# Performance work log

Measured on AMD Instinct MI355X. Metric: run time of the kernel, lower is better.

The kernel has to match this reference:

```python
import jax, jax.numpy as jnp
import numpy as np

N, K, CIN, COUT = 150000, 27, 128, 128


def setup_inputs() -> dict:
    key = jax.random.key(0)
    k1, k2, k3 = jax.random.split(key, 3)
    data = jax.random.normal(k1, (N, CIN), dtype=jnp.float32)
    weights = jax.random.normal(k2, (COUT, K, CIN), dtype=jnp.float32) * 0.05
    # neighbour indices in [-1, N): -1 marks empty octree neighbours (~1/151 here)
    neighbour = jax.random.randint(k3, (N, K), 0, N + 1, dtype=jnp.int64) - 1
    return {"data": data, "weights": weights, "neighbour": neighbour}


def reference(data, weights, neighbour):
    """Octree sparse conv: out[m] = sum_k W[:,k,:] @ data[neigh[m,k]] (0 if -1).

    Scans over the 27 kernel offsets so the [N,K,Cin] gather is never
    materialized; each step is a masked row-gather + dense GEMM.
    """
    w_k = jnp.transpose(weights, (1, 2, 0))   # [K, Cin, Cout]
    n_k = neighbour.T                          # [K, N]

    def body(acc, xs):
        w, idx = xs                            # [Cin, Cout], [N]
        valid = (idx >= 0)[:, None]            # [N, 1]
        g = jnp.where(valid, data[jnp.clip(idx, 0, None)], 0.0)  # [N, Cin]
        return acc + g @ w, None

    out0 = jnp.zeros((data.shape[0], w_k.shape[-1]), dtype=data.dtype)
    out, _ = jax.lax.scan(body, out0, (w_k, n_k))
    return out
```

## Files before the change

kernel.cpp:

```cpp
#include <hip/hip_runtime.h>

#define N_PTS 150000
#define NK 27
#define CIN 128
#define COUT 128
#define BM 256
#define NBLK ((N_PTS + BM - 1) / BM)

typedef __attribute__((ext_vector_type(8))) short bfrag8;
typedef __attribute__((ext_vector_type(4))) float facc4;

__device__ inline unsigned short f2bf(float f) {
    unsigned u = __builtin_bit_cast(unsigned, f);
    u += 0x7FFFu + ((u >> 16) & 1u);
    return (unsigned short)(u >> 16);
}
__device__ inline unsigned pack2(float a, float b) {
    return (unsigned)f2bf(a) | ((unsigned)f2bf(b) << 16);
}
__device__ inline void glds16(const void* g, void* l) {
    __builtin_amdgcn_global_load_lds(
        (const __attribute__((address_space(1))) void*)g,
        (__attribute__((address_space(3))) void*)l, 16, 0, 0);
}

__global__ void cast_data_kernel(const float* __restrict__ in,
                                 unsigned short* __restrict__ out) {
    const int n8_data = N_PTS * (CIN / 8);
    const int n8_all  = (N_PTS + 1) * (CIN / 8);
    int i = blockIdx.x * blockDim.x + threadIdx.x;
    int stride = gridDim.x * blockDim.x;
    for (; i < n8_all; i += stride) {
        uint4 v;
        if (i < n8_data) {
            const float4* p = (const float4*)(in + (size_t)i * 8);
            float4 x = p[0], y = p[1];
            v.x = pack2(x.x, x.y); v.y = pack2(x.z, x.w);
            v.z = pack2(y.x, y.y); v.w = pack2(y.z, y.w);
        } else {
            v.x = v.y = v.z = v.w = 0u;
        }
        *(uint4*)(out + (size_t)i * 8) = v;
    }
}

__global__ void prep_weights_h(const float* __restrict__ w,
                               unsigned short* __restrict__ wkh) {
    int i = blockIdx.x * blockDim.x + threadIdx.x;
    if (i >= NK * 2 * 128 * 8) return;
    int bu = i & 7, co = (i >> 3) & 127, h = (i >> 10) & 1, k = i >> 11;
    int ci = h * 64 + (bu ^ (co & 7)) * 8;
    const float4* src = (const float4*)(w + ((size_t)co * NK + k) * CIN + ci);
    float4 x = src[0], y = src[1];
    uint4 v;
    v.x = pack2(x.x, x.y); v.y = pack2(x.z, x.w);
    v.z = pack2(y.x, y.y); v.w = pack2(y.z, y.w);
    ((uint4*)wkh)[i] = v;
}


#define STAGE_A(Q, ADST)                                                     \
  {                                                                          \
    const int q_ = (Q);                                                      \
    const int k_ = q_ >> 1;                                                  \
    const int hb_ = (q_ & 1) << 7;                                           \
    int iv0 = *(const int*)(ldsI + i0base + k_ * 4);                         \
    int iv1 = *(const int*)(ldsI + i1base + k_ * 4);                         \
    size_t e0 = (r0ok && iv0 >= 0) ? (size_t)iv0 : (size_t)N_PTS;            \
    size_t e1 = (r1ok && iv1 >= 0) ? (size_t)iv1 : (size_t)N_PTS;            \
    glds16(dbfB + e0 * 256 + hb_ + aswz0, (ADST) + adst0);                   \
    glds16(dbfB + e1 * 256 + hb_ + aswz1, (ADST) + adst1);                   \
  }

#define STAGE_B(Q, BDST)                                                     \
    glds16(wkhB + (size_t)(Q) * 16384 + bsrc_c, (BDST) + bdst_lin);

#define MFMA_PHASE(ABUF, BBUF)                                                      \
  {                                                                                 \
    __builtin_amdgcn_s_setprio(1);                                                  \
    _Pragma("unroll")                                                               \
    for (int kk = 0; kk < 2; ++kk) {                                                \
      const int sw_ = (((kk * 4 + lk) ^ (lr & 7)) << 4);                            \
      bfrag8 a0 = *(const bfrag8*)((ABUF) + (wrow * 32 + lr) * 128 + sw_);          \
      bfrag8 a1 = *(const bfrag8*)((ABUF) + (wrow * 32 + 16 + lr) * 128 + sw_);     \
      _Pragma("unroll")                                                             \
      for (int ct = 0; ct < 4; ++ct) {                                              \
        bfrag8 b = *(const bfrag8*)((BBUF) + (h * 64 + ct * 16 + lr) * 128 + sw_);  \
        acc[0][ct] = __builtin_amdgcn_mfma_f32_16x16x32_bf16(a0, b, acc[0][ct],     \
                                                             0, 0, 0);              \
        acc[1][ct] = __builtin_amdgcn_mfma_f32_16x16x32_bf16(a1, b, acc[1][ct],     \
                                                             0, 0, 0);              \
      }                                                                             \
    }                                                                               \
    __builtin_amdgcn_s_setprio(0);                                                  \
  }

#define WAIT_BAR(N)                                                          \
    __builtin_amdgcn_sched_barrier(0);                                       \
    asm volatile("s_waitcnt vmcnt(" #N ")" ::: "memory");                    \
    __builtin_amdgcn_s_barrier();                                            \
    __builtin_amdgcn_sched_barrier(0);

__global__ __launch_bounds__(1024, 4)
void octconv_v8(const unsigned short* __restrict__ dbf,
                const unsigned short* __restrict__ wkh,
                const int* __restrict__ nbr,
                float* __restrict__ out) {
    __shared__ __align__(1024) unsigned char lds[3 * 32768 + 2 * 16384 + 27648];

    const int t = threadIdx.x;
    const int w = t >> 6, l = t & 63;
    const int lr = l & 15, lk = l >> 4;
    const int h = w & 1, wrow = w >> 1;
    const int m0 = blockIdx.x * BM;

    const int lu    = l & 7;
    const int slot0 = w * 16 + (l >> 3);
    const int slot1 = slot0 + 8;
    const bool r0ok = (m0 + slot0) < N_PTS;
    const bool r1ok = (m0 + slot1) < N_PTS;
    const int aswz0 = (lu ^ (slot0 & 7)) << 4;
    const int aswz1 = (lu ^ (slot1 & 7)) << 4;
    const int adst0 = slot0 * 128 + lu * 16;
    const int adst1 = slot1 * 128 + lu * 16;
    const int bsrc_c = t * 16;
    const int bdst_lin = t * 16;
    const int i0base = slot0 * 108;
    const int i1base = slot1 * 108;

    const char* dbfB = (const char*)dbf;
    const char* wkhB = (const char*)wkh;
    char* a0p = (char*)lds;
    char* a1p = (char*)lds + 32768;
    char* a2p = (char*)lds + 65536;
    char* b0p = (char*)lds + 98304;
    char* b1p = (char*)lds + 114688;
    char* ldsI = (char*)lds + 131072;

    facc4 acc[2][4];
    const facc4 fz = {0.f, 0.f, 0.f, 0.f};
#pragma unroll
    for (int a = 0; a < 2; ++a)
#pragma unroll
        for (int b = 0; b < 4; ++b) acc[a][b] = fz;

    {
        const char* nsrc = (const char*)nbr + (size_t)m0 * 108;
        const int rows_valid = (N_PTS - m0) < BM ? (N_PTS - m0) : BM;
        const int nlimit = rows_valid * 108;
        int o1 = t * 16;
        if (o1 < nlimit) glds16(nsrc + o1, ldsI + o1);
        int o2 = 16384 + t * 16;
        if (t < 704 && o2 < nlimit) glds16(nsrc + o2, ldsI + o2);
    }
    WAIT_BAR(0)

    STAGE_A(0, a0p)
    STAGE_B(0, b0p)
    STAGE_A(1, a1p)
    STAGE_B(1, b1p)
    WAIT_BAR(3)

    STAGE_A(2, a2p)
    MFMA_PHASE(a0p, b0p)
    WAIT_BAR(2)
    { char* tp = a0p; a0p = a1p; a1p = a2p; a2p = tp; }
    { char* tp = b0p; b0p = b1p; b1p = tp; }

#pragma unroll 1
    for (int p = 1; p <= 51; ++p) {
        STAGE_B(p + 1, b1p)
        STAGE_A(p + 2, a2p)
        MFMA_PHASE(a0p, b0p)
        WAIT_BAR(2)
        { char* tp = a0p; a0p = a1p; a1p = a2p; a2p = tp; }
        { char* tp = b0p; b0p = b1p; b1p = tp; }
    }

    STAGE_B(53, b1p)
    MFMA_PHASE(a0p, b0p)
    WAIT_BAR(0)
    { char* tp = a0p; a0p = a1p; a1p = a2p; a2p = tp; }
    { char* tp = b0p; b0p = b1p; b1p = tp; }

    MFMA_PHASE(a0p, b0p)

#pragma unroll
    for (int rt = 0; rt < 2; ++rt) {
        const int r0 = m0 + wrow * 32 + rt * 16 + lk * 4;
#pragma unroll
        for (int ct = 0; ct < 4; ++ct) {
#pragma unroll
            for (int r = 0; r < 4; ++r) {
                int row = r0 + r;
                if (row < N_PTS)
                    out[(size_t)row * COUT + h * 64 + ct * 16 + lr] = acc[rt][ct][r];
            }
        }
    }
}

__global__ void naive_kernel(const float* __restrict__ data, const float* __restrict__ wgt,
                             const int* __restrict__ nbr, float* __restrict__ out) {
    int mm = blockIdx.x;
    int co = threadIdx.x;
    if (mm >= N_PTS) return;
    float acc = 0.f;
    for (int k = 0; k < NK; ++k) {
        int idx = nbr[mm * NK + k];
        if (idx < 0) continue;
        const float* d  = data + (size_t)idx * CIN;
        const float* wp = wgt + ((size_t)co * NK + k) * CIN;
        for (int ci = 0; ci < CIN; ++ci) acc += d[ci] * wp[ci];
    }
    out[(size_t)mm * COUT + co] = acc;
}

extern "C" void kernel_launch(void* const* d_in, const int* in_sizes, int n_in,
                              void* d_out, int out_size, void* d_ws, size_t ws_size,
                              hipStream_t stream) {
    const float* data = (const float*)d_in[0];
    const float* wgt  = (const float*)d_in[1];
    const int*   nbr  = (const int*)d_in[2];
    float*       out  = (float*)d_out;

    const size_t wk_bytes  = (size_t)NK * 2 * 128 * 8 * 16;
    const size_t dbf_bytes = (size_t)(N_PTS + 1) * CIN * 2;

    if (ws_size < wk_bytes + dbf_bytes) {
        naive_kernel<<<N_PTS, COUT, 0, stream>>>(data, wgt, nbr, out);
        return;
    }
    unsigned short* wkh = (unsigned short*)d_ws;
    unsigned short* dbf = (unsigned short*)((char*)d_ws + wk_bytes);

    prep_weights_h<<<(NK * 2 * 128 * 8 + 255) / 256, 256, 0, stream>>>(wgt, wkh);
    cast_data_kernel<<<2048, 256, 0, stream>>>(data, dbf);

    octconv_v8<<<NBLK, 1024, 0, stream>>>(dbf, wkh, nbr, out);
}
```

Before: 197.2 us.

## Halve block threads and give each wave a 64x64 output tile

The conv kernel now launches 512 threads (8 waves) per 256-row block instead of 1024. Each wave computes four 16-row MFMA tiles instead of two, so every B fragment read from LDS feeds twice as many MFMAs. Each thread issues twice as many async global-to-LDS loads per stage, and the vmcnt waits are adjusted to match. This aims to cut LDS traffic per MFMA and wave scheduling overhead, at the cost of more accumulator registers and less latency hiding from fewer resident waves.

```diff
diff --git a/kernel.cpp b/kernel.cpp
--- a/kernel.cpp
+++ b/kernel.cpp
@@ -61,19 +61,28 @@
 
 #define STAGE_A(Q, ADST)                                                     \
   {                                                                          \
-    const int q_ = (Q);                                                      \
-    const int k_ = q_ >> 1;                                                  \
-    const int hb_ = (q_ & 1) << 7;                                           \
-    int iv0 = *(const int*)(ldsI + i0base + k_ * 4);                         \
-    int iv1 = *(const int*)(ldsI + i1base + k_ * 4);                         \
-    size_t e0 = (r0ok && iv0 >= 0) ? (size_t)iv0 : (size_t)N_PTS;            \
-    size_t e1 = (r1ok && iv1 >= 0) ? (size_t)iv1 : (size_t)N_PTS;            \
-    glds16(dbfB + e0 * 256 + hb_ + aswz0, (ADST) + adst0);                   \
-    glds16(dbfB + e1 * 256 + hb_ + aswz1, (ADST) + adst1);                   \
+    const int k_  = (Q) >> 1;                                                \
+    const int hb_ = ((Q) & 1) << 7;                                          \
+    int iv0 = *(const int*)(ldsI + s0 * 108 + k_ * 4);                       \
+    int iv1 = *(const int*)(ldsI + s1 * 108 + k_ * 4);                       \
+    int iv2 = *(const int*)(ldsI + s2 * 108 + k_ * 4);                       \
+    int iv3 = *(const int*)(ldsI + s3 * 108 + k_ * 4);                       \
+    size_t e0 = (s0ok && iv0 >= 0) ? (size_t)iv0 : (size_t)N_PTS;            \
+    size_t e1 = (s1ok && iv1 >= 0) ? (size_t)iv1 : (size_t)N_PTS;            \
+    size_t e2 = (s2ok && iv2 >= 0) ? (size_t)iv2 : (size_t)N_PTS;            \
+    size_t e3 = (s3ok && iv3 >= 0) ? (size_t)iv3 : (size_t)N_PTS;            \
+    glds16(dbfB + e0 * 256 + hb_ + aswz, (ADST) + s0 * 128 + lu16);          \
+    glds16(dbfB + e1 * 256 + hb_ + aswz, (ADST) + s1 * 128 + lu16);          \
+    glds16(dbfB + e2 * 256 + hb_ + aswz, (ADST) + s2 * 128 + lu16);          \
+    glds16(dbfB + e3 * 256 + hb_ + aswz, (ADST) + s3 * 128 + lu16);          \
   }
 
 #define STAGE_B(Q, BDST)                                                     \
-    glds16(wkhB + (size_t)(Q) * 16384 + bsrc_c, (BDST) + bdst_lin);
+  {                                                                          \
+    const char* bs_ = wkhB + (size_t)(Q) * 16384 + t * 16;                   \
+    glds16(bs_,        (BDST) + t * 16);                                     \
+    glds16(bs_ + 8192, (BDST) + t * 16 + 8192);                              \
+  }
 
 #define MFMA_PHASE(ABUF, BBUF)                                                      \
   {                                                                                 \
@@ -81,14 +90,20 @@
     _Pragma("unroll")                                                               \
     for (int kk = 0; kk < 2; ++kk) {                                                \
       const int sw_ = (((kk * 4 + lk) ^ (lr & 7)) << 4);                            \
-      bfrag8 a0 = *(const bfrag8*)((ABUF) + (wrow * 32 + lr) * 128 + sw_);          \
-      bfrag8 a1 = *(const bfrag8*)((ABUF) + (wrow * 32 + 16 + lr) * 128 + sw_);     \
+      bfrag8 a0 = *(const bfrag8*)((ABUF) + (wrow * 64 + lr) * 128 + sw_);          \
+      bfrag8 a1 = *(const bfrag8*)((ABUF) + (wrow * 64 + 16 + lr) * 128 + sw_);     \
+      bfrag8 a2 = *(const bfrag8*)((ABUF) + (wrow * 64 + 32 + lr) * 128 + sw_);     \
+      bfrag8 a3 = *(const bfrag8*)((ABUF) + (wrow * 64 + 48 + lr) * 128 + sw_);     \
       _Pragma("unroll")                                                             \
       for (int ct = 0; ct < 4; ++ct) {                                              \
         bfrag8 b = *(const bfrag8*)((BBUF) + (h * 64 + ct * 16 + lr) * 128 + sw_);  \
         acc[0][ct] = __builtin_amdgcn_mfma_f32_16x16x32_bf16(a0, b, acc[0][ct],     \
                                                              0, 0, 0);              \
         acc[1][ct] = __builtin_amdgcn_mfma_f32_16x16x32_bf16(a1, b, acc[1][ct],     \
+                                                             0, 0, 0);              \
+        acc[2][ct] = __builtin_amdgcn_mfma_f32_16x16x32_bf16(a2, b, acc[2][ct],     \
+                                                             0, 0, 0);              \
+        acc[3][ct] = __builtin_amdgcn_mfma_f32_16x16x32_bf16(a3, b, acc[3][ct],     \
                                                              0, 0, 0);              \
       }                                                                             \
     }                                                                               \
@@ -101,8 +116,8 @@
     __builtin_amdgcn_s_barrier();                                            \
     __builtin_amdgcn_sched_barrier(0);
 
-__global__ __launch_bounds__(1024, 4)
-void octconv_v8(const unsigned short* __restrict__ dbf,
+__global__ __launch_bounds__(512, 2)
+void octconv_v9(const unsigned short* __restrict__ dbf,
                 const unsigned short* __restrict__ wkh,
                 const int* __restrict__ nbr,
                 float* __restrict__ out) {
@@ -114,19 +129,15 @@
     const int h = w & 1, wrow = w >> 1;
     const int m0 = blockIdx.x * BM;
 
-    const int lu    = l & 7;
-    const int slot0 = w * 16 + (l >> 3);
-    const int slot1 = slot0 + 8;
-    const bool r0ok = (m0 + slot0) < N_PTS;
-    const bool r1ok = (m0 + slot1) < N_PTS;
-    const int aswz0 = (lu ^ (slot0 & 7)) << 4;
-    const int aswz1 = (lu ^ (slot1 & 7)) << 4;
-    const int adst0 = slot0 * 128 + lu * 16;
-    const int adst1 = slot1 * 128 + lu * 16;
-    const int bsrc_c = t * 16;
-    const int bdst_lin = t * 16;
-    const int i0base = slot0 * 108;
-    const int i1base = slot1 * 108;
+    const int lu   = l & 7;
+    const int lu16 = lu * 16;
+    const int sb   = w * 8 + (l >> 3);
+    const int s0 = sb, s1 = sb + 64, s2 = sb + 128, s3 = sb + 192;
+    const bool s0ok = (m0 + s0) < N_PTS;
+    const bool s1ok = (m0 + s1) < N_PTS;
+    const bool s2ok = (m0 + s2) < N_PTS;
+    const bool s3ok = (m0 + s3) < N_PTS;
+    const int aswz = (lu ^ (sb & 7)) << 4;
 
     const char* dbfB = (const char*)dbf;
     const char* wkhB = (const char*)wkh;
@@ -137,10 +148,10 @@
     char* b1p = (char*)lds + 114688;
     char* ldsI = (char*)lds + 131072;
 
-    facc4 acc[2][4];
+    facc4 acc[4][4];
     const facc4 fz = {0.f, 0.f, 0.f, 0.f};
 #pragma unroll
-    for (int a = 0; a < 2; ++a)
+    for (int a = 0; a < 4; ++a)
 #pragma unroll
         for (int b = 0; b < 4; ++b) acc[a][b] = fz;
 
@@ -148,10 +159,11 @@
         const char* nsrc = (const char*)nbr + (size_t)m0 * 108;
         const int rows_valid = (N_PTS - m0) < BM ? (N_PTS - m0) : BM;
         const int nlimit = rows_valid * 108;
-        int o1 = t * 16;
-        if (o1 < nlimit) glds16(nsrc + o1, ldsI + o1);
-        int o2 = 16384 + t * 16;
-        if (t < 704 && o2 < nlimit) glds16(nsrc + o2, ldsI + o2);
+        int o;
+        o = t * 16;         if (o < nlimit) glds16(nsrc + o, ldsI + o);
+        o = 8192 + t * 16;  if (o < nlimit) glds16(nsrc + o, ldsI + o);
+        o = 16384 + t * 16; if (o < nlimit) glds16(nsrc + o, ldsI + o);
+        o = 24576 + t * 16; if (t < 192 && o < nlimit) glds16(nsrc + o, ldsI + o);
     }
     WAIT_BAR(0)
 
@@ -159,11 +171,11 @@
     STAGE_B(0, b0p)
     STAGE_A(1, a1p)
     STAGE_B(1, b1p)
-    WAIT_BAR(3)
+    WAIT_BAR(6)
 
     STAGE_A(2, a2p)
     MFMA_PHASE(a0p, b0p)
-    WAIT_BAR(2)
+    WAIT_BAR(4)
     { char* tp = a0p; a0p = a1p; a1p = a2p; a2p = tp; }
     { char* tp = b0p; b0p = b1p; b1p = tp; }
 
@@ -172,7 +184,7 @@
         STAGE_B(p + 1, b1p)
         STAGE_A(p + 2, a2p)
         MFMA_PHASE(a0p, b0p)
-        WAIT_BAR(2)
+        WAIT_BAR(4)
         { char* tp = a0p; a0p = a1p; a1p = a2p; a2p = tp; }
         { char* tp = b0p; b0p = b1p; b1p = tp; }
     }
@@ -186,8 +198,8 @@
     MFMA_PHASE(a0p, b0p)
 
 #pragma unroll
-    for (int rt = 0; rt < 2; ++rt) {
-        const int r0 = m0 + wrow * 32 + rt * 16 + lk * 4;
+    for (int rt = 0; rt < 4; ++rt) {
+        const int r0 = m0 + wrow * 64 + rt * 16 + lk * 4;
 #pragma unroll
         for (int ct = 0; ct < 4; ++ct) {
 #pragma unroll
@@ -237,5 +249,5 @@
     prep_weights_h<<<(NK * 2 * 128 * 8 + 255) / 256, 256, 0, stream>>>(wgt, wkh);
     cast_data_kernel<<<2048, 256, 0, stream>>>(data, dbf);
 
-    octconv_v8<<<NBLK, 1024, 0, stream>>>(dbf, wkh, nbr, out);
-}
+    octconv_v9<<<NBLK, 512, 0, stream>>>(dbf, wkh, nbr, out);
+}
```

Result: slower. 204.5 us (+3.7%).
